# Kernel optimization log

Measured on AMD Instinct MI355X. Metric: run time of the kernel, lower is better.

The kernel has to match this reference:

```python
import jax, jax.numpy as jnp
import numpy as np


def setup_inputs() -> dict:
    key = jax.random.key(0)
    k1, k2, k3 = jax.random.split(key, 3)
    N = 16384
    y = jax.random.normal(k1, (N,), dtype=jnp.float32)
    y_hat = jax.random.normal(k2, (N,), dtype=jnp.float32)
    status = jax.random.randint(k3, (N,), 0, 2, dtype=jnp.int32)
    return {"y": y, "y_hat": y_hat, "status": status}


def reference(y, y_hat, status):
    # Pairwise concordance index over all pairs i < j.
    # ge[i, j] = y[i] >= y[j]; le[i, j] = y[i] <= y[j]
    N = y.shape[0]
    ge = y[:, None] >= y[None, :]
    le = y[:, None] <= y[None, :]
    ge_hat = y_hat[:, None] >= y_hat[None, :]
    le_hat = y_hat[:, None] <= y_hat[None, :]
    st_i = (status == 1)[:, None]  # astatus_1 broadcast over j
    st_j = (status == 1)[None, :]  # bstatus_1 broadcast over i
    # upper-triangular mask (strict): pairs with j > i
    mask = jnp.triu(jnp.ones((N, N), dtype=bool), k=1)

    c1 = ge & ge_hat & st_j
    c2 = le & le_hat & st_i
    cc = (c1 | c2) & mask

    tp1 = le & st_i
    tp2 = ge & st_j
    tp = (tp1 | tp2) & mask

    c = jnp.sum(cc.astype(jnp.int32)).astype(jnp.float32)
    total_pairs = jnp.sum(tp.astype(jnp.int32)).astype(jnp.float32)
    return c / total_pairs
```

## Files before the change

### kernel.cpp

```cpp
#include <hip/hip_runtime.h>


#define BLOCK 256
#define GRID  1024
#define RAWJ  512
#define TI    512

__global__ __launch_bounds__(BLOCK, 4) void cindex_one(
    const float* __restrict__ y, const float* __restrict__ yh,
    const int* __restrict__ status, int n,
    unsigned* __restrict__ ws, float* __restrict__ out)
{
    __shared__ __align__(16) float2 s_yy[RAWJ];
    __shared__ unsigned s_cnt, s_jc;
    __shared__ unsigned rA[4], rB[4];
    __shared__ int s_win;

    const int tid  = threadIdx.x;
    const int b    = blockIdx.x;
    const int lane = tid & 63;
    const int wav  = tid >> 6;

    const float PINF = __int_as_float(0x7f800000);
    const float NINF = __int_as_float(0xff800000);

    const int ntJ  = (n + RAWJ - 1) / RAWJ;
    const int ntI  = (n + TI - 1) / TI;
    const int ntot = ntI * ntJ;

    const unsigned ref = ws[0];

    unsigned bg = 0, bc = 0;

    for (int t = b; t < ntot; t += GRID) {
        const int ti = t / ntJ;
        const int tj = t - ti * ntJ;

        if (tid == 0) s_cnt = 0;
        __syncthreads();

        const int jr0 = tj * RAWJ + tid;
#pragma unroll
        for (int r = 0; r < RAWJ / BLOCK; ++r) {
            const int jr = jr0 + r * BLOCK;
            if (jr < n && status[jr] == 1) {
                unsigned p = atomicAdd(&s_cnt, 1u);
                s_yy[p] = make_float2(y[jr], yh[jr]);
            }
        }
        __syncthreads();
        if (tid < 8) {
            unsigned jc  = s_cnt;
            unsigned jcp = (jc + 7u) & ~7u;
            unsigned idx = jc + (unsigned)tid;
            if (idx < jcp) s_yy[idx] = make_float2(PINF, PINF);
            if (tid == 0) s_jc = jcp;
        }
        __syncthreads();
        const int jcnt = (int)s_jc;

        if (ti == 0 && tid == 0) {
            atomicAdd(&ws[1552 + 16 * (tj & 31)], s_cnt);
        }

        const int i0 = ti * TI + tid;
        const int i1 = i0 + BLOCK;
        const float yi0 = (i0 < n) ? y[i0]  : NINF;
        const float hh0 = (i0 < n) ? yh[i0] : NINF;
        const float yi1 = (i1 < n) ? y[i1]  : NINF;
        const float hh1 = (i1 < n) ? yh[i1] : NINF;

        for (int jj = 0; jj < jcnt; jj += 8) {
#pragma unroll
            for (int k = 0; k < 8; ++k) {
                float2 p = s_yy[jj + k];
                bool g0 = yi0 >= p.x, h0 = hh0 >= p.y;
                bool g1 = yi1 >= p.x, h1 = hh1 >= p.y;
                bg += (unsigned)g0 + (unsigned)g1;
                bc += (unsigned)(g0 & h0) + (unsigned)(g1 & h1);
            }
        }
        __syncthreads();
    }

#pragma unroll
    for (int off = 32; off > 0; off >>= 1) {
        bg += __shfl_down(bg, off, 64);
        bc += __shfl_down(bc, off, 64);
    }
    if (lane == 0) { rA[wav] = bg; rB[wav] = bc; }
    __syncthreads();

    if (tid == 0) {
        unsigned tg = rA[0] + rA[1] + rA[2] + rA[3];
        unsigned tc = rB[0] + rB[1] + rB[2] + rB[3];
        unsigned o1 = atomicAdd(&ws[528  + 16 * (b & 31)], tg);
        unsigned o2 = atomicAdd(&ws[1040 + 16 * (b & 31)], tc);
        asm volatile("" :: "v"(o1), "v"(o2));
        asm volatile("s_waitcnt vmcnt(0)" ::: "memory");
        int winflag = 0;
        unsigned og = atomicAdd(&ws[16 + 16 * (b & 31)], 1u);
        if (og - ref == (unsigned)(GRID / 32 - 1)) {
            unsigned os = atomicAdd(&ws[2064], 1u);
            winflag = (os - ref == 31u) ? 1 : 0;
        }
        s_win = winflag;
    }
    __syncthreads();

    if (s_win) {
        unsigned sg = 0, sc = 0, sk = 0;
        if (tid < 32) {
            sg = atomicAdd(&ws[528  + 16 * tid], 0u);
            sc = atomicAdd(&ws[1040 + 16 * tid], 0u);
            sk = atomicAdd(&ws[1552 + 16 * tid], 0u);
        }
#pragma unroll
        for (int off = 32; off > 0; off >>= 1) {
            sg += __shfl_down(sg, off, 64);
            sc += __shfl_down(sc, off, 64);
            sk += __shfl_down(sk, off, 64);
        }
        if (tid == 0) {
            unsigned T1 = sg - 32u * ref;
            unsigned S1 = sc - 32u * ref;
            unsigned K  = sk - 32u * ref;
            long long cn = (long long)S1 - (long long)K;
            long long tn = (long long)T1 - (long long)K;
            out[0] = (float)cn / (float)tn;
        }
    }
}

extern "C" void kernel_launch(void* const* d_in, const int* in_sizes, int n_in,
                              void* d_out, int out_size, void* d_ws, size_t ws_size,
                              hipStream_t stream) {
    const float* y      = (const float*)d_in[0];
    const float* y_hat  = (const float*)d_in[1];
    const int*   status = (const int*)d_in[2];
    float* out = (float*)d_out;
    int n = in_sizes[0];
    unsigned* ws = (unsigned*)d_ws;

    hipLaunchKernelGGL(cindex_one, dim3(GRID), dim3(BLOCK), 0, stream,
                       y, y_hat, status, n, ws, out);
}
```

Before: 79.57 us.

## Use wave ballots for stream compaction and for pair counting

Replaces the shared-memory atomic compaction of status==1 elements with a ballot/popcount prefix scheme, which preserves the original order and removes the LDS atomics. The inner comparison loop now turns each compare into a wave-wide ballot mask and accumulates popcounts, so every lane holds the wave total and the final shuffle reduction is dropped. The ballot results are scalar values, so the counting is meant to move from per-lane vector adds to scalar popcount and add work. The cost is four ballots per pair element plus extra barriers in the compaction loop.

```diff
diff --git a/kernel.cpp b/kernel.cpp
--- a/kernel.cpp
+++ b/kernel.cpp
@@ -12,7 +12,7 @@
     unsigned* __restrict__ ws, float* __restrict__ out)
 {
     __shared__ __align__(16) float2 s_yy[RAWJ];
-    __shared__ unsigned s_cnt, s_jc;
+    __shared__ unsigned wcnt[4];
     __shared__ unsigned rA[4], rB[4];
     __shared__ int s_win;
 
@@ -36,32 +36,36 @@
         const int ti = t / ntJ;
         const int tj = t - ti * ntJ;
 
-        if (tid == 0) s_cnt = 0;
-        __syncthreads();
-
-        const int jr0 = tj * RAWJ + tid;
+        unsigned fill = 0;
 #pragma unroll
         for (int r = 0; r < RAWJ / BLOCK; ++r) {
-            const int jr = jr0 + r * BLOCK;
-            if (jr < n && status[jr] == 1) {
-                unsigned p = atomicAdd(&s_cnt, 1u);
-                s_yy[p] = make_float2(y[jr], yh[jr]);
+            const int jr = tj * RAWJ + r * BLOCK + tid;
+            const bool st = (jr < n) && (status[jr] == 1);
+            unsigned long long m = __ballot(st);
+            if (lane == 0) wcnt[wav] = (unsigned)__popcll(m);
+            __syncthreads();
+            unsigned woff = fill;
+            for (int w = 0; w < wav; ++w) woff += wcnt[w];
+            if (st) {
+                const unsigned long long lt =
+                    (lane == 63) ? (~0ull >> 1) : ((1ull << lane) - 1ull);
+                unsigned pos = woff + (unsigned)__popcll(m & lt);
+                s_yy[pos] = make_float2(y[jr], yh[jr]);
             }
+            fill += wcnt[0] + wcnt[1] + wcnt[2] + wcnt[3];
+            __syncthreads();
+        }
+
+        const unsigned jcp = (fill + 7u) & ~7u;
+        if (tid < 8) {
+            unsigned idx = fill + (unsigned)tid;
+            if (idx < jcp) s_yy[idx] = make_float2(PINF, PINF);
+        }
+        if (ti == 0 && tid == 0) {
+            atomicAdd(&ws[1552 + 16 * (tj & 31)], fill);
         }
         __syncthreads();
-        if (tid < 8) {
-            unsigned jc  = s_cnt;
-            unsigned jcp = (jc + 7u) & ~7u;
-            unsigned idx = jc + (unsigned)tid;
-            if (idx < jcp) s_yy[idx] = make_float2(PINF, PINF);
-            if (tid == 0) s_jc = jcp;
-        }
-        __syncthreads();
-        const int jcnt = (int)s_jc;
-
-        if (ti == 0 && tid == 0) {
-            atomicAdd(&ws[1552 + 16 * (tj & 31)], s_cnt);
-        }
+        const int jcnt = (int)jcp;
 
         const int i0 = ti * TI + tid;
         const int i1 = i0 + BLOCK;
@@ -74,20 +78,17 @@
 #pragma unroll
             for (int k = 0; k < 8; ++k) {
                 float2 p = s_yy[jj + k];
-                bool g0 = yi0 >= p.x, h0 = hh0 >= p.y;
-                bool g1 = yi1 >= p.x, h1 = hh1 >= p.y;
-                bg += (unsigned)g0 + (unsigned)g1;
-                bc += (unsigned)(g0 & h0) + (unsigned)(g1 & h1);
+                unsigned long long g0 = __ballot(yi0 >= p.x);
+                unsigned long long h0 = __ballot(hh0 >= p.y);
+                unsigned long long g1 = __ballot(yi1 >= p.x);
+                unsigned long long h1 = __ballot(hh1 >= p.y);
+                bg += (unsigned)__popcll(g0) + (unsigned)__popcll(g1);
+                bc += (unsigned)__popcll(g0 & h0) + (unsigned)__popcll(g1 & h1);
             }
         }
         __syncthreads();
     }
 
-#pragma unroll
-    for (int off = 32; off > 0; off >>= 1) {
-        bg += __shfl_down(bg, off, 64);
-        bc += __shfl_down(bc, off, 64);
-    }
     if (lane == 0) { rA[wav] = bg; rB[wav] = bc; }
     __syncthreads();
 
```

Result: slower. 86.80 us (+9.1%).
